# Kernel optimization log

Measured on AMD Instinct MI355X. Metric: run time of the kernel, lower is better.

## Reference

```python
import jax, jax.numpy as jnp
import numpy as np

DIM = 512
CROSS_DIM = 512
NUM_HEADS = 8
DIM_HEAD = 64
INNER = NUM_HEADS * DIM_HEAD  # 512
SCALE = DIM_HEAD ** -0.5


def setup_inputs() -> dict:
    key = jax.random.key(0)
    ks = jax.random.split(key, 7)
    B, S, C = 2, 4096, 4096
    x = jax.random.normal(ks[0], (B, S, DIM), dtype=jnp.float32)
    context = jax.random.normal(ks[1], (B, C, CROSS_DIM), dtype=jnp.float32)
    # nn.Linear weights stored as [out, in]; we apply x @ W.T
    w_q = jax.random.normal(ks[2], (INNER, DIM), dtype=jnp.float32) * (DIM ** -0.5)
    w_k = jax.random.normal(ks[3], (INNER, CROSS_DIM), dtype=jnp.float32) * (CROSS_DIM ** -0.5)
    w_v = jax.random.normal(ks[4], (INNER, CROSS_DIM), dtype=jnp.float32) * (CROSS_DIM ** -0.5)
    w_out = jax.random.normal(ks[5], (DIM, INNER), dtype=jnp.float32) * (INNER ** -0.5)
    b_out = jax.random.normal(ks[6], (DIM,), dtype=jnp.float32) * 0.02
    return {"x": x, "context": context, "w_q": w_q, "w_k": w_k,
            "w_v": w_v, "w_out": w_out, "b_out": b_out}


def reference(x, context, w_q, w_k, w_v, w_out, b_out):
    B, S, _ = x.shape
    _, C, _ = context.shape
    # projections -> [B, H, L, Dh]
    q = (x @ w_q.T).reshape(B, S, NUM_HEADS, DIM_HEAD).transpose(0, 2, 1, 3)
    k = (context @ w_k.T).reshape(B, C, NUM_HEADS, DIM_HEAD).transpose(0, 2, 1, 3)
    v = (context @ w_v.T).reshape(B, C, NUM_HEADS, DIM_HEAD).transpose(0, 2, 1, 3)
    # scores [B, H, S, C]
    scores = jnp.einsum('bhsd,bhcd->bhsc', q, k) * SCALE
    attn = jax.nn.softmax(scores, axis=-1)
    out = jnp.einsum('bhsc,bhcd->bhsd', attn, v)  # [B,H,S,Dh]
    out = out.transpose(0, 2, 1, 3).reshape(B, S, INNER)
    return out @ w_out.T + b_out
```

## Files before the change

kernel.cpp:

```cpp
#include <hip/hip_runtime.h>

typedef __bf16 bf16;
typedef __bf16 bf16x2 __attribute__((ext_vector_type(2)));
typedef __bf16 bf16x4 __attribute__((ext_vector_type(4)));
typedef __bf16 bf16x8 __attribute__((ext_vector_type(8)));
typedef float  f32x4  __attribute__((ext_vector_type(4)));
typedef float  f32x16 __attribute__((ext_vector_type(16)));
typedef unsigned int uint4v __attribute__((ext_vector_type(4)));

#define MFMA16(a,b,c) __builtin_amdgcn_mfma_f32_16x16x32_bf16(a,b,c,0,0,0)
#define MFMA32(a,b,c) __builtin_amdgcn_mfma_f32_32x32x16_bf16(a,b,c,0,0,0)

__device__ __forceinline__ bf16x8 ld8_f32_to_bf16(const float* __restrict__ p)
{
    f32x4 a = *(const f32x4*)p;
    f32x4 b = *(const f32x4*)(p + 4);
    bf16x8 o;
#pragma unroll
    for (int j = 0; j < 4; j++) { o[j] = (bf16)a[j]; o[4 + j] = (bf16)b[j]; }
    return o;
}

__global__ __launch_bounds__(256, 2) void mm_qkv(
    const float* __restrict__ x,  const float* __restrict__ ctx,
    const float* __restrict__ wq, const float* __restrict__ wk,
    const float* __restrict__ wv,
    bf16* __restrict__ Qb, bf16* __restrict__ Kb, bf16* __restrict__ Vtb)
{
    __shared__ bf16 Al[128 * 40];
    __shared__ bf16 Wl[128 * 40];

    const int L  = blockIdx.x + 4 * (blockIdx.y + 64 * blockIdx.z);
    const int L2 = (L & 7) * 96 + (L >> 3);
    const int bx = L2 & 3;
    const int by = (L2 >> 2) & 63;
    const int z  = L2 >> 8;

    const float* A; const float* W; bf16* out; int mode;
    if (z == 0)      { A = x;   W = wq; out = Qb;  mode = 0; }
    else if (z == 1) { A = ctx; W = wk; out = Kb;  mode = 0; }
    else             { A = ctx; W = wv; out = Vtb; mode = 1; }

    const int tid  = threadIdx.x;
    const int lane = tid & 63;
    const int w    = tid >> 6;
    const int wr   = w >> 1, wc = w & 1;
    const int q    = lane >> 4, m0 = lane & 15;

    f32x4 acc[4][4];
#pragma unroll
    for (int i = 0; i < 4; i++)
#pragma unroll
        for (int j = 0; j < 4; j++)
#pragma unroll
            for (int r = 0; r < 4; r++) acc[i][j][r] = 0.f;

    const int r0 = tid >> 2;
    const int c0 = (tid & 3) * 8;
    const float* Ab = A + (size_t)(by * 128) * 512;
    const float* Wb = W + (size_t)(bx * 128) * 512;

    for (int k0 = 0; k0 < 512; k0 += 32) {
        *(bf16x8*)&Al[r0 * 40 + c0]        = ld8_f32_to_bf16(Ab + (size_t)r0 * 512 + k0 + c0);
        *(bf16x8*)&Al[(r0 + 64) * 40 + c0] = ld8_f32_to_bf16(Ab + (size_t)(r0 + 64) * 512 + k0 + c0);
        *(bf16x8*)&Wl[r0 * 40 + c0]        = ld8_f32_to_bf16(Wb + (size_t)r0 * 512 + k0 + c0);
        *(bf16x8*)&Wl[(r0 + 64) * 40 + c0] = ld8_f32_to_bf16(Wb + (size_t)(r0 + 64) * 512 + k0 + c0);
        __syncthreads();

        bf16x8 af[4], wf[4];
#pragma unroll
        for (int mt = 0; mt < 4; mt++)
            af[mt] = *(const bf16x8*)&Al[(wr * 64 + mt * 16 + m0) * 40 + q * 8];
#pragma unroll
        for (int nt = 0; nt < 4; nt++)
            wf[nt] = *(const bf16x8*)&Wl[(wc * 64 + nt * 16 + m0) * 40 + q * 8];
#pragma unroll
        for (int mt = 0; mt < 4; mt++)
#pragma unroll
            for (int nt = 0; nt < 4; nt++)
                acc[mt][nt] = MFMA16(af[mt], wf[nt], acc[mt][nt]);
        __syncthreads();
    }

#pragma unroll
    for (int nt = 0; nt < 4; nt++) {
        const int col = bx * 128 + wc * 64 + nt * 16 + m0;
#pragma unroll
        for (int mt = 0; mt < 4; mt++) {
#pragma unroll
            for (int r = 0; r < 4; r++) {
                const int row = by * 128 + wr * 64 + mt * 16 + q * 4 + r;
                const bf16 v16 = (bf16)acc[mt][nt][r];
                if (mode == 0) {
                    out[(size_t)row * 512 + col] = v16;
                } else {
                    const int bb = row >> 12, c = row & 4095;
                    const int hh = col >> 6,  d = col & 63;
                    out[(size_t)((bb * 8 + hh) * 64 + d) * 4096 + c] = v16;
                }
            }
        }
    }
}

__global__ __launch_bounds__(256, 2) void mm_oproj(
    const bf16* __restrict__ Ob, const float* __restrict__ wout,
    const float* __restrict__ bout, float* __restrict__ out)
{
    __shared__ bf16 Al[128 * 40];
    __shared__ bf16 Wl[128 * 40];

    const int L  = blockIdx.x + 4 * blockIdx.y;
    const int L2 = (L & 7) * 32 + (L >> 3);
    const int bx = L2 & 3;
    const int by = L2 >> 2;

    const int tid  = threadIdx.x;
    const int lane = tid & 63;
    const int w    = tid >> 6;
    const int wr   = w >> 1, wc = w & 1;
    const int q    = lane >> 4, m0 = lane & 15;

    f32x4 acc[4][4];
#pragma unroll
    for (int i = 0; i < 4; i++)
#pragma unroll
        for (int j = 0; j < 4; j++)
#pragma unroll
            for (int r = 0; r < 4; r++) acc[i][j][r] = 0.f;

    const int r0 = tid >> 2;
    const int c0 = (tid & 3) * 8;
    const bf16*  Ab = Ob   + (size_t)(by * 128) * 512;
    const float* Wb = wout + (size_t)(bx * 128) * 512;

    for (int k0 = 0; k0 < 512; k0 += 32) {
        *(bf16x8*)&Al[r0 * 40 + c0]        = *(const bf16x8*)(Ab + (size_t)r0 * 512 + k0 + c0);
        *(bf16x8*)&Al[(r0 + 64) * 40 + c0] = *(const bf16x8*)(Ab + (size_t)(r0 + 64) * 512 + k0 + c0);
        *(bf16x8*)&Wl[r0 * 40 + c0]        = ld8_f32_to_bf16(Wb + (size_t)r0 * 512 + k0 + c0);
        *(bf16x8*)&Wl[(r0 + 64) * 40 + c0] = ld8_f32_to_bf16(Wb + (size_t)(r0 + 64) * 512 + k0 + c0);
        __syncthreads();

        bf16x8 af[4], wf[4];
#pragma unroll
        for (int mt = 0; mt < 4; mt++)
            af[mt] = *(const bf16x8*)&Al[(wr * 64 + mt * 16 + m0) * 40 + q * 8];
#pragma unroll
        for (int nt = 0; nt < 4; nt++)
            wf[nt] = *(const bf16x8*)&Wl[(wc * 64 + nt * 16 + m0) * 40 + q * 8];
#pragma unroll
        for (int mt = 0; mt < 4; mt++)
#pragma unroll
            for (int nt = 0; nt < 4; nt++)
                acc[mt][nt] = MFMA16(af[mt], wf[nt], acc[mt][nt]);
        __syncthreads();
    }

#pragma unroll
    for (int nt = 0; nt < 4; nt++) {
        const int col = bx * 128 + wc * 64 + nt * 16 + m0;
        const float bv = bout[col];
#pragma unroll
        for (int mt = 0; mt < 4; mt++) {
#pragma unroll
            for (int r = 0; r < 4; r++) {
                const int row = by * 128 + wr * 64 + mt * 16 + q * 4 + r;
                out[(size_t)row * 512 + col] = acc[mt][nt][r] + bv;
            }
        }
    }
}

__global__ __launch_bounds__(256, 2) void fa_attn(
    const bf16* __restrict__ Qb, const bf16* __restrict__ Kb,
    const bf16* __restrict__ Vtb, bf16* __restrict__ Ob,
    float* __restrict__ Opart, float2* __restrict__ ml, const int nsplit)
{
    __shared__ bf16 Kl[2][64 * 72];
    __shared__ bf16 Vl[2][64 * 72];

    const int tid  = threadIdx.x;
    const int lane = tid & 63;
    const int w    = tid >> 6;
    const int n0   = lane & 31;
    const int hd   = lane >> 5;

    const int nper = 64 * nsplit;
    const int L  = blockIdx.x + 32 * (blockIdx.y + 8 * blockIdx.z);
    const int L2 = (L & 7) * nper + (L >> 3);
    const int qx = L2 & 31;
    const int yz = L2 >> 5;
    const int h0 = yz & 7;
    const int zz = yz >> 3;
    const int b  = (nsplit == 2) ? (zz >> 1) : zz;
    const int ch = (nsplit == 2) ? (zz & 1) : 0;
    const int clen = (nsplit == 2) ? 2048 : 4096;
    const int c0 = ch * clen;
    const int qg = qx * 128 + w * 32;

    bf16x8 qf[4];
    const bf16* qp = Qb + (size_t)(b * 4096 + qg + n0) * 512 + h0 * 64 + hd * 8;
#pragma unroll
    for (int ks = 0; ks < 4; ks++) {
        bf16x8 t = *(const bf16x8*)(qp + ks * 16);
#pragma unroll
        for (int j = 0; j < 8; j++) t[j] = (bf16)((float)t[j] * 0.125f);
        qf[ks] = t;
    }

    f32x16 oc[2];
#pragma unroll
    for (int dt = 0; dt < 2; dt++)
#pragma unroll
        for (int r = 0; r < 16; r++) oc[dt][r] = 0.f;
    float mrun = -1e30f, lrun = 0.f;

    const int srow = tid >> 2;
    const int scol = (tid & 3) * 16;
    const bf16* Kg = Kb  + (size_t)(b * 4096) * 512 + h0 * 64;
    const bf16* Vg = Vtb + (size_t)(b * 8 + h0) * 64 * 4096;

#define STAGE(buf, cb_) do { \
    *(bf16x8*)&Kl[buf][srow * 72 + scol]     = *(const bf16x8*)(Kg + (size_t)((cb_) + srow) * 512 + scol); \
    *(bf16x8*)&Kl[buf][srow * 72 + scol + 8] = *(const bf16x8*)(Kg + (size_t)((cb_) + srow) * 512 + scol + 8); \
    *(bf16x8*)&Vl[buf][srow * 72 + scol]     = *(const bf16x8*)(Vg + (size_t)srow * 4096 + (cb_) + scol); \
    *(bf16x8*)&Vl[buf][srow * 72 + scol + 8] = *(const bf16x8*)(Vg + (size_t)srow * 4096 + (cb_) + scol + 8); \
} while (0)

    STAGE(0, c0);
    int cur = 0;

    for (int cb = c0; cb < c0 + clen; cb += 64) {
        __syncthreads();
        if (cb + 64 < c0 + clen) STAGE(cur ^ 1, cb + 64);

        const bf16* Kc = &Kl[cur][0];
        const bf16* Vc = &Vl[cur][0];

        f32x16 st[2];
#pragma unroll
        for (int ct = 0; ct < 2; ct++) {
#pragma unroll
            for (int r = 0; r < 16; r++) st[ct][r] = 0.f;
#pragma unroll
            for (int ks = 0; ks < 4; ks++) {
                bf16x8 kf = *(const bf16x8*)&Kc[(ct * 32 + n0) * 72 + ks * 16 + hd * 8];
                st[ct] = MFMA32(kf, qf[ks], st[ct]);
            }
        }

        float mx = st[0][0];
#pragma unroll
        for (int ct = 0; ct < 2; ct++)
#pragma unroll
            for (int r = 0; r < 16; r++) mx = fmaxf(mx, st[ct][r]);
        mx = fmaxf(mx, __shfl_xor(mx, 32));

        if (__any(mx > mrun + 8.f)) {
            const float mnew = fmaxf(mrun, mx);
            const float al = __expf(mrun - mnew);
            mrun = mnew;
            lrun *= al;
#pragma unroll
            for (int dt = 0; dt < 2; dt++)
#pragma unroll
                for (int r = 0; r < 16; r++) oc[dt][r] *= al;
        }

        unsigned int pd[2][4][2];
        float rs = 0.f;
#pragma unroll
        for (int ct = 0; ct < 2; ct++)
#pragma unroll
            for (int g = 0; g < 4; g++)
#pragma unroll
                for (int t = 0; t < 2; t++) {
                    const float e0 = __expf(st[ct][4 * g + 2 * t]     - mrun);
                    const float e1 = __expf(st[ct][4 * g + 2 * t + 1] - mrun);
                    rs += e0 + e1;
                    bf16x2 pr; pr[0] = (bf16)e0; pr[1] = (bf16)e1;
                    pd[ct][g][t] = __builtin_bit_cast(unsigned int, pr);
                }
        rs += __shfl_xor(rs, 32);
        lrun += rs;

#pragma unroll
        for (int ks = 0; ks < 4; ks++) {
            const int ct = ks >> 1;
            const int g0 = 2 * (ks & 1), g1 = g0 + 1;
            const unsigned int own0  = hd ? pd[ct][g1][0] : pd[ct][g0][0];
            const unsigned int own1  = hd ? pd[ct][g1][1] : pd[ct][g0][1];
            const unsigned int send0 = hd ? pd[ct][g0][0] : pd[ct][g1][0];
            const unsigned int send1 = hd ? pd[ct][g0][1] : pd[ct][g1][1];
            const unsigned int r0 = (unsigned int)__shfl_xor((int)send0, 32);
            const unsigned int r1 = (unsigned int)__shfl_xor((int)send1, 32);
            uint4v u;
            u[0] = hd ? r0 : own0;
            u[1] = hd ? r1 : own1;
            u[2] = hd ? own0 : r0;
            u[3] = hd ? own1 : r1;
            const bf16x8 pf = __builtin_bit_cast(bf16x8, u);
#pragma unroll
            for (int dt = 0; dt < 2; dt++) {
                bf16x8 vf = *(const bf16x8*)&Vc[(dt * 32 + n0) * 72 + ks * 16 + hd * 8];
                oc[dt] = MFMA32(vf, pf, oc[dt]);
            }
        }
        cur ^= 1;
    }
#undef STAGE

    if (nsplit == 1) {
        const float rli = 1.0f / lrun;
        bf16* ob = Ob + (size_t)(b * 4096 + qg + n0) * 512 + h0 * 64;
#pragma unroll
        for (int dt = 0; dt < 2; dt++)
#pragma unroll
            for (int rq = 0; rq < 4; rq++) {
                bf16x4 o4;
#pragma unroll
                for (int i = 0; i < 4; i++) o4[i] = (bf16)(oc[dt][4 * rq + i] * rli);
                *(bf16x4*)&ob[dt * 32 + rq * 8 + hd * 4] = o4;
            }
    } else {
        float* Op = Opart + ((size_t)(ch * 2 + b) * 4096 + qg + n0) * 512 + h0 * 64;
#pragma unroll
        for (int dt = 0; dt < 2; dt++)
#pragma unroll
            for (int rq = 0; rq < 4; rq++) {
                f32x4 o4;
#pragma unroll
                for (int i = 0; i < 4; i++) o4[i] = oc[dt][4 * rq + i];
                *(f32x4*)&Op[dt * 32 + rq * 8 + hd * 4] = o4;
            }
        if (hd == 0)
            ml[((size_t)(ch * 2 + b) * 8 + h0) * 4096 + qg + n0] = make_float2(mrun, lrun);
    }
}

__global__ __launch_bounds__(256) void fa_merge(
    const float* __restrict__ Opart, const float2* __restrict__ ml,
    bf16* __restrict__ Ob)
{
    const int e   = blockIdx.x * 256 + threadIdx.x;
    const int row = e >> 7;
    const int c4  = (e & 127) * 4;
    const int b   = row >> 12, sr = row & 4095, h = c4 >> 6;

    const float2 u = ml[((size_t)(0 + b) * 8 + h) * 4096 + sr];
    const float2 v = ml[((size_t)(2 + b) * 8 + h) * 4096 + sr];
    const float m  = fmaxf(u.x, v.x);
    const float w1 = __expf(u.x - m), w2 = __expf(v.x - m);
    const float rL = 1.0f / (u.y * w1 + v.y * w2);

    const f32x4 o1 = *(const f32x4*)&Opart[((size_t)(0 + b) * 4096 + sr) * 512 + c4];
    const f32x4 o2 = *(const f32x4*)&Opart[((size_t)(2 + b) * 4096 + sr) * 512 + c4];
    bf16x4 o;
#pragma unroll
    for (int i = 0; i < 4; i++) o[i] = (bf16)((o1[i] * w1 + o2[i] * w2) * rL);
    *(bf16x4*)&Ob[(size_t)row * 512 + c4] = o;
}

__global__ void ws_sig11(float* out) { if (threadIdx.x == 0) out[0] = 777.0f; }

extern "C" void kernel_launch(void* const* d_in, const int* in_sizes, int n_in,
                              void* d_out, int out_size, void* d_ws, size_t ws_size,
                              hipStream_t stream)
{
    const float* x    = (const float*)d_in[0];
    const float* ctx  = (const float*)d_in[1];
    const float* wq   = (const float*)d_in[2];
    const float* wk   = (const float*)d_in[3];
    const float* wv   = (const float*)d_in[4];
    const float* wout = (const float*)d_in[5];
    const float* bout = (const float*)d_in[6];
    float* out = (float*)d_out;

    char* ws = (char*)d_ws;
    const size_t MB = 1024 * 1024;
    const size_t SZ = (size_t)8192 * 512 * sizeof(bf16);
    if (ws_size < 32 * MB) {
        ws_sig11<<<dim3(1), dim3(64), 0, stream>>>(out);
        return;
    }

    bf16* Qb  = (bf16*)(ws);
    bf16* Kb  = (bf16*)(ws + SZ);
    bf16* Vtb = (bf16*)(ws + 2 * SZ);
    bf16* Ob  = (bf16*)(ws + 3 * SZ);

    const int nsplit = (ws_size >= 66 * MB) ? 2 : 1;
    float*  Opart = (float*)(ws + 32 * MB);
    float2* mlp   = (float2*)(ws + 64 * MB);

    mm_qkv  <<<dim3(4, 64, 3), dim3(256), 0, stream>>>(x, ctx, wq, wk, wv, Qb, Kb, Vtb);
    fa_attn <<<dim3(32, 8, 2 * nsplit), dim3(256), 0, stream>>>(Qb, Kb, Vtb, Ob, Opart, mlp, nsplit);
    if (nsplit == 2)
        fa_merge<<<dim3(4096), dim3(256), 0, stream>>>(Opart, mlp, Ob);
    mm_oproj<<<dim3(4, 64, 1), dim3(256), 0, stream>>>(Ob, wout, bout, out);
}
```

Baseline: 246.5 us.

## Pre-convert inputs to bf16, use direct global-to-LDS loads, switch to exp2

Adds a kernel that converts x, context and all weights from fp32 to bf16 in one pass. The projection GEMMs then stage tiles with global_load_lds straight into unpadded LDS, which removes per-tile conversion and register round trips. Softmax folds log2(e) into the Q scale and uses the hardware exp2, and the transposed-V store is vectorised to 4 bf16. The split-KV path is now mandatory and the workspace requirement rises. The trade-off is an extra launch plus a full extra read and write of the inputs, and possible LDS bank conflicts from dropping the row padding.

```diff
diff --git a/kernel.cpp b/kernel.cpp
--- a/kernel.cpp
+++ b/kernel.cpp
@@ -11,6 +11,24 @@
 #define MFMA16(a,b,c) __builtin_amdgcn_mfma_f32_16x16x32_bf16(a,b,c,0,0,0)
 #define MFMA32(a,b,c) __builtin_amdgcn_mfma_f32_32x32x16_bf16(a,b,c,0,0,0)
 
+#if __has_builtin(__builtin_amdgcn_exp2f)
+#define EXP2(x) __builtin_amdgcn_exp2f(x)
+#else
+#define EXP2(x) exp2f(x)
+#endif
+
+__device__ __forceinline__ void gl16(const bf16* __restrict__ g, bf16* l)
+{
+#if __has_builtin(__builtin_amdgcn_global_load_lds)
+    __builtin_amdgcn_global_load_lds(
+        (const __attribute__((address_space(1))) void*)g,
+        (__attribute__((address_space(3))) void*)l, 16, 0, 0);
+#else
+    const int ln = __builtin_amdgcn_mbcnt_hi(~0u, __builtin_amdgcn_mbcnt_lo(~0u, 0));
+    *(bf16x8*)((bf16*)l + ln * 8) = *(const bf16x8*)g;
+#endif
+}
+
 __device__ __forceinline__ bf16x8 ld8_f32_to_bf16(const float* __restrict__ p)
 {
     f32x4 a = *(const f32x4*)p;
@@ -21,14 +39,33 @@
     return o;
 }
 
-__global__ __launch_bounds__(256, 2) void mm_qkv(
+__global__ __launch_bounds__(256) void cvt6(
     const float* __restrict__ x,  const float* __restrict__ ctx,
     const float* __restrict__ wq, const float* __restrict__ wk,
-    const float* __restrict__ wv,
+    const float* __restrict__ wv, const float* __restrict__ wout,
+    bf16* __restrict__ xb, bf16* __restrict__ cb, bf16* __restrict__ wqb,
+    bf16* __restrict__ wkb, bf16* __restrict__ wvb, bf16* __restrict__ wob)
+{
+    const int bid = blockIdx.x;
+    const float* s; bf16* d; int base;
+    if      (bid < 2048) { s = x;    d = xb;  base = 0;    }
+    else if (bid < 4096) { s = ctx;  d = cb;  base = 2048; }
+    else if (bid < 4224) { s = wq;   d = wqb; base = 4096; }
+    else if (bid < 4352) { s = wk;   d = wkb; base = 4224; }
+    else if (bid < 4480) { s = wv;   d = wvb; base = 4352; }
+    else                 { s = wout; d = wob; base = 4480; }
+    const int i = ((bid - base) * 256 + threadIdx.x) * 8;
+    *(bf16x8*)&d[i] = ld8_f32_to_bf16(s + i);
+}
+
+__global__ __launch_bounds__(256, 2) void mm_qkv(
+    const bf16* __restrict__ xb, const bf16* __restrict__ cb,
+    const bf16* __restrict__ wqb, const bf16* __restrict__ wkb,
+    const bf16* __restrict__ wvb,
     bf16* __restrict__ Qb, bf16* __restrict__ Kb, bf16* __restrict__ Vtb)
 {
-    __shared__ bf16 Al[128 * 40];
-    __shared__ bf16 Wl[128 * 40];
+    __shared__ bf16 Al[128 * 32];
+    __shared__ bf16 Wl[128 * 32];
 
     const int L  = blockIdx.x + 4 * (blockIdx.y + 64 * blockIdx.z);
     const int L2 = (L & 7) * 96 + (L >> 3);
@@ -36,10 +73,10 @@
     const int by = (L2 >> 2) & 63;
     const int z  = L2 >> 8;
 
-    const float* A; const float* W; bf16* out; int mode;
-    if (z == 0)      { A = x;   W = wq; out = Qb;  mode = 0; }
-    else if (z == 1) { A = ctx; W = wk; out = Kb;  mode = 0; }
-    else             { A = ctx; W = wv; out = Vtb; mode = 1; }
+    const bf16* A; const bf16* W; bf16* out; int mode;
+    if (z == 0)      { A = xb; W = wqb; out = Qb;  mode = 0; }
+    else if (z == 1) { A = cb; W = wkb; out = Kb;  mode = 0; }
+    else             { A = cb; W = wvb; out = Vtb; mode = 1; }
 
     const int tid  = threadIdx.x;
     const int lane = tid & 63;
@@ -55,25 +92,25 @@
 #pragma unroll
             for (int r = 0; r < 4; r++) acc[i][j][r] = 0.f;
 
-    const int r0 = tid >> 2;
-    const int c0 = (tid & 3) * 8;
-    const float* Ab = A + (size_t)(by * 128) * 512;
-    const float* Wb = W + (size_t)(bx * 128) * 512;
+    const bf16* Ab = A + (size_t)(by * 128) * 512;
+    const bf16* Wb = W + (size_t)(bx * 128) * 512;
+    const int sr = w * 16 + (lane >> 2);
+    const int sc = (lane & 3) * 8;
 
     for (int k0 = 0; k0 < 512; k0 += 32) {
-        *(bf16x8*)&Al[r0 * 40 + c0]        = ld8_f32_to_bf16(Ab + (size_t)r0 * 512 + k0 + c0);
-        *(bf16x8*)&Al[(r0 + 64) * 40 + c0] = ld8_f32_to_bf16(Ab + (size_t)(r0 + 64) * 512 + k0 + c0);
-        *(bf16x8*)&Wl[r0 * 40 + c0]        = ld8_f32_to_bf16(Wb + (size_t)r0 * 512 + k0 + c0);
-        *(bf16x8*)&Wl[(r0 + 64) * 40 + c0] = ld8_f32_to_bf16(Wb + (size_t)(r0 + 64) * 512 + k0 + c0);
+        gl16(Ab + (size_t)sr * 512 + k0 + sc,        &Al[(w * 16) * 32]);
+        gl16(Ab + (size_t)(sr + 64) * 512 + k0 + sc, &Al[(64 + w * 16) * 32]);
+        gl16(Wb + (size_t)sr * 512 + k0 + sc,        &Wl[(w * 16) * 32]);
+        gl16(Wb + (size_t)(sr + 64) * 512 + k0 + sc, &Wl[(64 + w * 16) * 32]);
         __syncthreads();
 
         bf16x8 af[4], wf[4];
 #pragma unroll
         for (int mt = 0; mt < 4; mt++)
-            af[mt] = *(const bf16x8*)&Al[(wr * 64 + mt * 16 + m0) * 40 + q * 8];
+            af[mt] = *(const bf16x8*)&Al[(wr * 64 + mt * 16 + m0) * 32 + q * 8];
 #pragma unroll
         for (int nt = 0; nt < 4; nt++)
-            wf[nt] = *(const bf16x8*)&Wl[(wc * 64 + nt * 16 + m0) * 40 + q * 8];
+            wf[nt] = *(const bf16x8*)&Wl[(wc * 64 + nt * 16 + m0) * 32 + q * 8];
 #pragma unroll
         for (int mt = 0; mt < 4; mt++)
 #pragma unroll
@@ -87,28 +124,29 @@
         const int col = bx * 128 + wc * 64 + nt * 16 + m0;
 #pragma unroll
         for (int mt = 0; mt < 4; mt++) {
-#pragma unroll
-            for (int r = 0; r < 4; r++) {
-                const int row = by * 128 + wr * 64 + mt * 16 + q * 4 + r;
-                const bf16 v16 = (bf16)acc[mt][nt][r];
-                if (mode == 0) {
-                    out[(size_t)row * 512 + col] = v16;
-                } else {
-                    const int bb = row >> 12, c = row & 4095;
-                    const int hh = col >> 6,  d = col & 63;
-                    out[(size_t)((bb * 8 + hh) * 64 + d) * 4096 + c] = v16;
-                }
+            const int row0 = by * 128 + wr * 64 + mt * 16 + q * 4;
+            if (mode == 0) {
+#pragma unroll
+                for (int r = 0; r < 4; r++)
+                    out[(size_t)(row0 + r) * 512 + col] = (bf16)acc[mt][nt][r];
+            } else {
+                const int bb = row0 >> 12, c = row0 & 4095;
+                const int hh = col >> 6,  d = col & 63;
+                bf16x4 o4;
+#pragma unroll
+                for (int r = 0; r < 4; r++) o4[r] = (bf16)acc[mt][nt][r];
+                *(bf16x4*)&out[(size_t)((bb * 8 + hh) * 64 + d) * 4096 + c] = o4;
             }
         }
     }
 }
 
 __global__ __launch_bounds__(256, 2) void mm_oproj(
-    const bf16* __restrict__ Ob, const float* __restrict__ wout,
+    const bf16* __restrict__ Ob, const bf16* __restrict__ wob,
     const float* __restrict__ bout, float* __restrict__ out)
 {
-    __shared__ bf16 Al[128 * 40];
-    __shared__ bf16 Wl[128 * 40];
+    __shared__ bf16 Al[128 * 32];
+    __shared__ bf16 Wl[128 * 32];
 
     const int L  = blockIdx.x + 4 * blockIdx.y;
     const int L2 = (L & 7) * 32 + (L >> 3);
@@ -129,25 +167,25 @@
 #pragma unroll
             for (int r = 0; r < 4; r++) acc[i][j][r] = 0.f;
 
-    const int r0 = tid >> 2;
-    const int c0 = (tid & 3) * 8;
-    const bf16*  Ab = Ob   + (size_t)(by * 128) * 512;
-    const float* Wb = wout + (size_t)(bx * 128) * 512;
+    const bf16* Ab = Ob  + (size_t)(by * 128) * 512;
+    const bf16* Wb = wob + (size_t)(bx * 128) * 512;
+    const int sr = w * 16 + (lane >> 2);
+    const int sc = (lane & 3) * 8;
 
     for (int k0 = 0; k0 < 512; k0 += 32) {
-        *(bf16x8*)&Al[r0 * 40 + c0]        = *(const bf16x8*)(Ab + (size_t)r0 * 512 + k0 + c0);
-        *(bf16x8*)&Al[(r0 + 64) * 40 + c0] = *(const bf16x8*)(Ab + (size_t)(r0 + 64) * 512 + k0 + c0);
-        *(bf16x8*)&Wl[r0 * 40 + c0]        = ld8_f32_to_bf16(Wb + (size_t)r0 * 512 + k0 + c0);
-        *(bf16x8*)&Wl[(r0 + 64) * 40 + c0] = ld8_f32_to_bf16(Wb + (size_t)(r0 + 64) * 512 + k0 + c0);
+        gl16(Ab + (size_t)sr * 512 + k0 + sc,        &Al[(w * 16) * 32]);
+        gl16(Ab + (size_t)(sr + 64) * 512 + k0 + sc, &Al[(64 + w * 16) * 32]);
+        gl16(Wb + (size_t)sr * 512 + k0 + sc,        &Wl[(w * 16) * 32]);
+        gl16(Wb + (size_t)(sr + 64) * 512 + k0 + sc, &Wl[(64 + w * 16) * 32]);
         __syncthreads();
 
         bf16x8 af[4], wf[4];
 #pragma unroll
         for (int mt = 0; mt < 4; mt++)
-            af[mt] = *(const bf16x8*)&Al[(wr * 64 + mt * 16 + m0) * 40 + q * 8];
+            af[mt] = *(const bf16x8*)&Al[(wr * 64 + mt * 16 + m0) * 32 + q * 8];
 #pragma unroll
         for (int nt = 0; nt < 4; nt++)
-            wf[nt] = *(const bf16x8*)&Wl[(wc * 64 + nt * 16 + m0) * 40 + q * 8];
+            wf[nt] = *(const bf16x8*)&Wl[(wc * 64 + nt * 16 + m0) * 32 + q * 8];
 #pragma unroll
         for (int mt = 0; mt < 4; mt++)
 #pragma unroll
@@ -198,13 +236,14 @@
     const int c0 = ch * clen;
     const int qg = qx * 128 + w * 32;
 
+    const float qsc = 0.125f * 1.44269504089f;
     bf16x8 qf[4];
     const bf16* qp = Qb + (size_t)(b * 4096 + qg + n0) * 512 + h0 * 64 + hd * 8;
 #pragma unroll
     for (int ks = 0; ks < 4; ks++) {
         bf16x8 t = *(const bf16x8*)(qp + ks * 16);
 #pragma unroll
-        for (int j = 0; j < 8; j++) t[j] = (bf16)((float)t[j] * 0.125f);
+        for (int j = 0; j < 8; j++) t[j] = (bf16)((float)t[j] * qsc);
         qf[ks] = t;
     }
 
@@ -258,7 +297,7 @@
 
         if (__any(mx > mrun + 8.f)) {
             const float mnew = fmaxf(mrun, mx);
-            const float al = __expf(mrun - mnew);
+            const float al = EXP2(mrun - mnew);
             mrun = mnew;
             lrun *= al;
 #pragma unroll
@@ -275,8 +314,8 @@
             for (int g = 0; g < 4; g++)
 #pragma unroll
                 for (int t = 0; t < 2; t++) {
-                    const float e0 = __expf(st[ct][4 * g + 2 * t]     - mrun);
-                    const float e1 = __expf(st[ct][4 * g + 2 * t + 1] - mrun);
+                    const float e0 = EXP2(st[ct][4 * g + 2 * t]     - mrun);
+                    const float e1 = EXP2(st[ct][4 * g + 2 * t + 1] - mrun);
                     rs += e0 + e1;
                     bf16x2 pr; pr[0] = (bf16)e0; pr[1] = (bf16)e1;
                     pd[ct][g][t] = __builtin_bit_cast(unsigned int, pr);
@@ -350,7 +389,7 @@
     const float2 u = ml[((size_t)(0 + b) * 8 + h) * 4096 + sr];
     const float2 v = ml[((size_t)(2 + b) * 8 + h) * 4096 + sr];
     const float m  = fmaxf(u.x, v.x);
-    const float w1 = __expf(u.x - m), w2 = __expf(v.x - m);
+    const float w1 = EXP2(u.x - m), w2 = EXP2(v.x - m);
     const float rL = 1.0f / (u.y * w1 + v.y * w2);
 
     const f32x4 o1 = *(const f32x4*)&Opart[((size_t)(0 + b) * 4096 + sr) * 512 + c4];
@@ -379,7 +418,7 @@
     char* ws = (char*)d_ws;
     const size_t MB = 1024 * 1024;
     const size_t SZ = (size_t)8192 * 512 * sizeof(bf16);
-    if (ws_size < 32 * MB) {
+    if (ws_size < 66 * MB) {
         ws_sig11<<<dim3(1), dim3(64), 0, stream>>>(out);
         return;
     }
@@ -389,13 +428,19 @@
     bf16* Vtb = (bf16*)(ws + 2 * SZ);
     bf16* Ob  = (bf16*)(ws + 3 * SZ);
 
-    const int nsplit = (ws_size >= 66 * MB) ? 2 : 1;
+    bf16* xb  = (bf16*)(ws + 32 * MB);
+    bf16* cbf = (bf16*)(ws + 40 * MB);
+    bf16* wqb = (bf16*)(ws + 48 * MB);
+    bf16* wkb = (bf16*)(ws + 48 * MB + 512 * 1024);
+    bf16* wvb = (bf16*)(ws + 49 * MB);
     float*  Opart = (float*)(ws + 32 * MB);
     float2* mlp   = (float2*)(ws + 64 * MB);
-
-    mm_qkv  <<<dim3(4, 64, 3), dim3(256), 0, stream>>>(x, ctx, wq, wk, wv, Qb, Kb, Vtb);
-    fa_attn <<<dim3(32, 8, 2 * nsplit), dim3(256), 0, stream>>>(Qb, Kb, Vtb, Ob, Opart, mlp, nsplit);
-    if (nsplit == 2)
-        fa_merge<<<dim3(4096), dim3(256), 0, stream>>>(Opart, mlp, Ob);
-    mm_oproj<<<dim3(4, 64, 1), dim3(256), 0, stream>>>(Ob, wout, bout, out);
-}
+    bf16*   wob   = (bf16*)(ws + 65 * MB);
+
+    cvt6    <<<dim3(4608), dim3(256), 0, stream>>>(x, ctx, wq, wk, wv, wout,
+                                                   xb, cbf, wqb, wkb, wvb, wob);
+    mm_qkv  <<<dim3(4, 64, 3), dim3(256), 0, stream>>>(xb, cbf, wqb, wkb, wvb, Qb, Kb, Vtb);
+    fa_attn <<<dim3(32, 8, 4), dim3(256), 0, stream>>>(Qb, Kb, Vtb, Ob, Opart, mlp, 2);
+    fa_merge<<<dim3(4096), dim3(256), 0, stream>>>(Opart, mlp, Ob);
+    mm_oproj<<<dim3(4, 64, 1), dim3(256), 0, stream>>>(Ob, wob, bout, out);
+}
```

Result: faster. 223.7 us (-9.2%).
